# Optimization experiments

Measured on AMD Instinct MI355X. Metric: run time of the kernel, lower is better.

The kernel has to match this reference:

```python
import jax, jax.numpy as jnp
import numpy as np

T, N, M, B = 512, 512, 256, 256

def setup_inputs() -> dict:
    key = jax.random.key(0)
    ks = jax.random.split(key, 6)
    h_t = jax.random.normal(ks[0], (1, B, M), dtype=jnp.float32)
    s_t = jax.random.normal(ks[1], (1, B, M), dtype=jnp.float32)
    data = jax.random.normal(ks[2], (B, T, N), dtype=jnp.float32)
    # torch Linear weight layout: (out_features, in_features)
    W_e = jax.random.normal(ks[3], (T, 2 * M), dtype=jnp.float32) / np.sqrt(2 * M)
    U_e = jax.random.normal(ks[4], (T, T), dtype=jnp.float32) / np.sqrt(T)
    v_e = jax.random.normal(ks[5], (1, T), dtype=jnp.float32) / np.sqrt(T)
    return {"h_t": h_t, "s_t": s_t, "data": data, "W_e": W_e, "U_e": U_e, "v_e": v_e}

def reference(h_t, s_t, data, W_e, U_e, v_e):
    # h_t, s_t: (1, B, m) -> (B, 2m); query is identical across the n repeats,
    # so project once and broadcast instead of materializing (B, n, 2m).
    query = jnp.concatenate([h_t[0], s_t[0]], axis=-1)          # (B, 2m)
    wq = query @ W_e.T                                          # (B, T)
    ud = jnp.einsum('btn,st->bns', data, U_e)                   # (B, n, T)
    alpha = jnp.tanh(wq[:, None, :] + ud)                       # (B, n, T)
    scores = jnp.einsum('bnt,t->bn', alpha, v_e[0])             # (B, n)
    attn = jax.nn.softmax(scores, axis=-1)[:, None, :]          # (B, 1, n)
    return attn
```

## Files before the change

### kernel.cpp

```cpp
#include <hip/hip_runtime.h>
#include <hip/hip_bf16.h>
#include <cmath>

#define T_DIM 512
#define N_DIM 512
#define M_DIM 256
#define B_DIM 256

typedef __bf16 bf16x8 __attribute__((ext_vector_type(8)));
typedef float  f32x4  __attribute__((ext_vector_type(4)));
typedef unsigned int u32;

__device__ __forceinline__ void gload16(const __bf16* g, __bf16* l) {
    __builtin_amdgcn_global_load_lds(
        (const __attribute__((address_space(1))) void*)g,
        (__attribute__((address_space(3))) void*)l, 16, 0, 0);
}

__device__ __forceinline__ int bkey(int r) { return ((r >> 3) ^ (r >> 1)) & 3; }

__global__ __launch_bounds__(256) void uconv_kernel(
    const float* __restrict__ U, __bf16* __restrict__ Uh)
{
    const int i = (blockIdx.x * 256 + threadIdx.x) * 2;
    float2 v = *(const float2*)(U + i);
    Uh[i]   = (__bf16)v.x;
    Uh[i+1] = (__bf16)v.y;
}

__global__ __launch_bounds__(256) void wq_kernel(
    const float* __restrict__ h_t, const float* __restrict__ s_t,
    const float* __restrict__ W_e, float* __restrict__ wq)
{
    __shared__ float q[2 * M_DIM];
    const int b = blockIdx.x;
    const int tid = threadIdx.x;
    q[tid]         = h_t[(size_t)b * M_DIM + tid];
    q[M_DIM + tid] = s_t[(size_t)b * M_DIM + tid];
    __syncthreads();
    for (int tt = tid; tt < T_DIM; tt += 256) {
        const float4* wrow = (const float4*)(W_e + (size_t)tt * (2 * M_DIM));
        float acc = 0.f;
        #pragma unroll 4
        for (int k4 = 0; k4 < (2 * M_DIM) / 4; ++k4) {
            float4 w = wrow[k4];
            acc += q[4*k4+0] * w.x + q[4*k4+1] * w.y
                 + q[4*k4+2] * w.z + q[4*k4+3] * w.w;
        }
        wq[(size_t)b * T_DIM + tt] = acc;
    }
}

__global__ __launch_bounds__(256, 2) void fused7_kernel(
    const float* __restrict__ data, const __bf16* __restrict__ Uh,
    const float* __restrict__ v_e, const float* __restrict__ wq,
    float* __restrict__ partial)
{
    __shared__ __align__(16) __bf16 As[2][128 * 32];
    __shared__ __align__(16) __bf16 Bs[2][256 * 32];
    __shared__ float sc[128];

    const int wg    = blockIdx.x;
    const int xcd   = wg & 7;
    const int local = wg >> 3;
    const int sh    = local & 1;
    const int p     = xcd + 8 * (local >> 1);
    const int b     = p >> 2;
    const int nb    = p & 3;

    const int tid  = threadIdx.x;
    const int lane = tid & 63;
    const int wid  = tid >> 6;
    const int wm   = wid >> 1;
    const int wn   = wid & 1;

    if (tid < 128) sc[tid] = 0.f;

    f32x4 acc[4][8];
    const f32x4 zero = {0.f, 0.f, 0.f, 0.f};
    #pragma unroll
    for (int i = 0; i < 4; ++i)
        #pragma unroll
        for (int j = 0; j < 8; ++j)
            acc[i][j] = zero;

    const float*  Ab = data + (size_t)b * T_DIM * N_DIM + nb * 128;
    const __bf16* Bb = Uh + (size_t)(sh * 256) * T_DIM;

    const int rp = tid >> 4;
    const int cg = tid & 15;
    const int n0 = cg * 8;

    const int r0   = tid >> 2;
    const int keyB = bkey(r0);
    const int ce   = (((tid & 3) ^ keyB) * 8);

    const int fr = lane & 15;
    const int kb = (lane >> 4) * 8;

    int aoff[4];
    #pragma unroll
    for (int mi = 0; mi < 4; ++mi) {
        const int row = wm * 64 + mi * 16 + fr;
        aoff[mi] = row * 32 + (kb ^ (bkey(row) << 3));
    }
    int boff[8];
    #pragma unroll
    for (int ni = 0; ni < 8; ++ni) {
        const int row = wn * 128 + ni * 16 + fr;
        boff[ni] = row * 32 + (kb ^ (bkey(row) << 3));
    }

    const float* s0 = Ab + (size_t)(2 * rp) * N_DIM + n0;
    float4 pa0 = *(const float4*)s0;
    float4 pa1 = *(const float4*)(s0 + 4);
    float4 pa2 = *(const float4*)(s0 + N_DIM);
    float4 pa3 = *(const float4*)(s0 + N_DIM + 4);

    #pragma unroll
    for (int i = 0; i < 4; ++i)
        gload16(Bb + (size_t)(i * 64 + r0) * T_DIM + ce, &Bs[0][tid * 8] + i * 64 * 32);
    {
        u32* As32 = (u32*)As[0];
        const float lo_[8] = {pa0.x, pa0.y, pa0.z, pa0.w, pa1.x, pa1.y, pa1.z, pa1.w};
        const float hi_[8] = {pa2.x, pa2.y, pa2.z, pa2.w, pa3.x, pa3.y, pa3.z, pa3.w};
        #pragma unroll
        for (int j = 0; j < 8; ++j) {
            __bf16 l = (__bf16)lo_[j];
            __bf16 h = (__bf16)hi_[j];
            u32 w = ((u32)__builtin_bit_cast(unsigned short, h) << 16)
                  |  (u32)__builtin_bit_cast(unsigned short, l);
            const int key = (cg ^ (j >> 1)) & 3;
            As32[(n0 + j) * 16 + (rp ^ (key << 2))] = w;
        }
    }
    {
        const float* sn = Ab + (size_t)(32 + 2 * rp) * N_DIM + n0;
        pa0 = *(const float4*)sn;
        pa1 = *(const float4*)(sn + 4);
        pa2 = *(const float4*)(sn + N_DIM);
        pa3 = *(const float4*)(sn + N_DIM + 4);
    }
    __syncthreads();

    int cur = 0;
    for (int k0 = 0; k0 < T_DIM; k0 += 32) {
        bf16x8 a[4], bv[8];
        #pragma unroll
        for (int mi = 0; mi < 4; ++mi)
            a[mi] = *(const bf16x8*)&As[cur][aoff[mi]];
        #pragma unroll
        for (int ni = 0; ni < 8; ++ni)
            bv[ni] = *(const bf16x8*)&Bs[cur][boff[ni]];

        if (k0 + 32 < T_DIM) {
            const int nxt = cur ^ 1;
            #pragma unroll
            for (int i = 0; i < 4; ++i)
                gload16(Bb + (size_t)(i * 64 + r0) * T_DIM + (k0 + 32) + ce,
                        &Bs[nxt][tid * 8] + i * 64 * 32);
            u32* As32 = (u32*)As[nxt];
            const float lo_[8] = {pa0.x, pa0.y, pa0.z, pa0.w, pa1.x, pa1.y, pa1.z, pa1.w};
            const float hi_[8] = {pa2.x, pa2.y, pa2.z, pa2.w, pa3.x, pa3.y, pa3.z, pa3.w};
            #pragma unroll
            for (int j = 0; j < 8; ++j) {
                __bf16 l = (__bf16)lo_[j];
                __bf16 h = (__bf16)hi_[j];
                u32 w = ((u32)__builtin_bit_cast(unsigned short, h) << 16)
                      |  (u32)__builtin_bit_cast(unsigned short, l);
                const int key = (cg ^ (j >> 1)) & 3;
                As32[(n0 + j) * 16 + (rp ^ (key << 2))] = w;
            }
            if (k0 + 64 < T_DIM) {
                const float* sn = Ab + (size_t)(k0 + 64 + 2 * rp) * N_DIM + n0;
                pa0 = *(const float4*)sn;
                pa1 = *(const float4*)(sn + 4);
                pa2 = *(const float4*)(sn + N_DIM);
                pa3 = *(const float4*)(sn + N_DIM + 4);
            }
        }

        __builtin_amdgcn_s_setprio(1);
        #pragma unroll
        for (int mi = 0; mi < 4; ++mi)
            #pragma unroll
            for (int ni = 0; ni < 8; ++ni)
                acc[mi][ni] = __builtin_amdgcn_mfma_f32_16x16x32_bf16(a[mi], bv[ni], acc[mi][ni], 0, 0, 0);
        __builtin_amdgcn_s_setprio(0);

        __syncthreads();
        cur ^= 1;
    }

    float wqv[8], vev[8];
    #pragma unroll
    for (int ni = 0; ni < 8; ++ni) {
        const int scol = sh * 256 + wn * 128 + ni * 16 + fr;
        wqv[ni] = wq[(size_t)b * T_DIM + scol];
        vev[ni] = v_e[scol];
    }
    const int g = lane >> 4;
    #pragma unroll
    for (int mi = 0; mi < 4; ++mi) {
        #pragma unroll
        for (int rg = 0; rg < 4; ++rg) {
            float part = 0.f;
            #pragma unroll
            for (int ni = 0; ni < 8; ++ni)
                part += vev[ni] * tanhf(wqv[ni] + acc[mi][ni][rg]);
            part += __shfl_xor(part, 1);
            part += __shfl_xor(part, 2);
            part += __shfl_xor(part, 4);
            part += __shfl_xor(part, 8);
            if (fr == 0)
                atomicAdd(&sc[wm * 64 + mi * 16 + 4 * g + rg], part);
        }
    }
    __syncthreads();
    if (tid < 128)
        partial[((size_t)b * 2 + sh) * N_DIM + nb * 128 + tid] = sc[tid];
}

__global__ __launch_bounds__(512) void softmax_kernel(
    const float* __restrict__ partial, float* __restrict__ out)
{
    const int b = blockIdx.x;
    const int n = threadIdx.x;
    const float* p = partial + (size_t)b * 2 * N_DIM;
    float s = p[n] + p[N_DIM + n];

    float m = s;
    #pragma unroll
    for (int off = 1; off < 64; off <<= 1)
        m = fmaxf(m, __shfl_xor(m, off));
    __shared__ float red[8];
    const int wv = n >> 6;
    if ((n & 63) == 0) red[wv] = m;
    __syncthreads();
    float bm = red[0];
    #pragma unroll
    for (int i = 1; i < 8; ++i) bm = fmaxf(bm, red[i]);

    float e = expf(s - bm);
    float t = e;
    #pragma unroll
    for (int off = 1; off < 64; off <<= 1)
        t += __shfl_xor(t, off);
    __syncthreads();
    if ((n & 63) == 0) red[wv] = t;
    __syncthreads();
    float tot = 0.f;
    #pragma unroll
    for (int i = 0; i < 8; ++i) tot += red[i];

    out[(size_t)b * N_DIM + n] = e / tot;
}

extern "C" void kernel_launch(void* const* d_in, const int* in_sizes, int n_in,
                              void* d_out, int out_size, void* d_ws, size_t ws_size,
                              hipStream_t stream) {
    const float* h_t  = (const float*)d_in[0];
    const float* s_t  = (const float*)d_in[1];
    const float* data = (const float*)d_in[2];
    const float* W_e  = (const float*)d_in[3];
    const float* U_e  = (const float*)d_in[4];
    const float* v_e  = (const float*)d_in[5];
    float* out = (float*)d_out;

    const size_t wq_elems      = (size_t)B_DIM * T_DIM;
    const size_t partial_elems = (size_t)B_DIM * 2 * N_DIM;
    const size_t u_elems       = (size_t)T_DIM * T_DIM;

    float* wq      = (float*)d_ws;
    float* partial = wq + wq_elems;
    __bf16* Uh     = (__bf16*)(partial + partial_elems);

    wq_kernel<<<B_DIM, 256, 0, stream>>>(h_t, s_t, W_e, wq);
    uconv_kernel<<<(int)(u_elems / 512), 256, 0, stream>>>(U_e, Uh);
    fused7_kernel<<<B_DIM * 8, 256, 0, stream>>>(data, Uh, v_e, wq, partial);
    softmax_kernel<<<B_DIM, 512, 0, stream>>>(partial, out);
}
```

Measured before the change: 175.7 us.

## Make fused GEMM-tanh kernel persistent over four batches and use fast exp tanh

The main kernel now launches 512 workgroups, down from 2048. Each workgroup processes four consecutive batches in one continuous 64-step K loop, so the double-buffered prefetch runs across batch boundaries and the pipeline prologue is amortised. After every 16 steps it runs the tanh/v_e epilogue, writes partial scores, and resets the accumulators and the shared score buffer. tanhf is replaced by an __expf-based formula, which is cheaper but can lose accuracy or overflow to inf for large inputs. The cost is a smaller grid, which may leave compute units underused, and extra barriers inside the loop.

```diff
diff --git a/kernel.cpp b/kernel.cpp
--- a/kernel.cpp
+++ b/kernel.cpp
@@ -18,6 +18,10 @@
 }
 
 __device__ __forceinline__ int bkey(int r) { return ((r >> 3) ^ (r >> 1)) & 3; }
+
+__device__ __forceinline__ float ftanh(float x) {
+    return 1.f - 2.f / (__expf(2.f * x) + 1.f);
+}
 
 __global__ __launch_bounds__(256) void uconv_kernel(
     const float* __restrict__ U, __bf16* __restrict__ Uh)
@@ -51,7 +55,7 @@
     }
 }
 
-__global__ __launch_bounds__(256, 2) void fused7_kernel(
+__global__ __launch_bounds__(256, 2) void fused8_kernel(
     const float* __restrict__ data, const __bf16* __restrict__ Uh,
     const float* __restrict__ v_e, const float* __restrict__ wq,
     float* __restrict__ partial)
@@ -64,9 +68,9 @@
     const int xcd   = wg & 7;
     const int local = wg >> 3;
     const int sh    = local & 1;
-    const int p     = xcd + 8 * (local >> 1);
-    const int b     = p >> 2;
-    const int nb    = p & 3;
+    const int q     = xcd + 8 * (local >> 1);
+    const int bgrp  = q >> 2;
+    const int nb    = q & 3;
 
     const int tid  = threadIdx.x;
     const int lane = tid & 63;
@@ -84,13 +88,13 @@
         for (int j = 0; j < 8; ++j)
             acc[i][j] = zero;
 
-    const float*  Ab = data + (size_t)b * T_DIM * N_DIM + nb * 128;
-    const __bf16* Bb = Uh + (size_t)(sh * 256) * T_DIM;
-
     const int rp = tid >> 4;
     const int cg = tid & 15;
     const int n0 = cg * 8;
 
+    const float* Apan = data + ((size_t)bgrp * 4 * T_DIM) * N_DIM + nb * 128 + n0;
+
+    const __bf16* Bb = Uh + (size_t)(sh * 256) * T_DIM;
     const int r0   = tid >> 2;
     const int keyB = bkey(r0);
     const int ce   = (((tid & 3) ^ keyB) * 8);
@@ -111,12 +115,20 @@
         boff[ni] = row * 32 + (kb ^ (bkey(row) << 3));
     }
 
-    const float* s0 = Ab + (size_t)(2 * rp) * N_DIM + n0;
-    float4 pa0 = *(const float4*)s0;
-    float4 pa1 = *(const float4*)(s0 + 4);
-    float4 pa2 = *(const float4*)(s0 + N_DIM);
-    float4 pa3 = *(const float4*)(s0 + N_DIM + 4);
-
+    float vev[8];
+    #pragma unroll
+    for (int ni = 0; ni < 8; ++ni)
+        vev[ni] = v_e[sh * 256 + wn * 128 + ni * 16 + fr];
+    const int g = lane >> 4;
+
+    float4 pa0, pa1, pa2, pa3;
+    {
+        const float* s0 = Apan + (size_t)(2 * rp) * N_DIM;
+        pa0 = *(const float4*)s0;
+        pa1 = *(const float4*)(s0 + 4);
+        pa2 = *(const float4*)(s0 + N_DIM);
+        pa3 = *(const float4*)(s0 + N_DIM + 4);
+    }
     #pragma unroll
     for (int i = 0; i < 4; ++i)
         gload16(Bb + (size_t)(i * 64 + r0) * T_DIM + ce, &Bs[0][tid * 8] + i * 64 * 32);
@@ -135,7 +147,7 @@
         }
     }
     {
-        const float* sn = Ab + (size_t)(32 + 2 * rp) * N_DIM + n0;
+        const float* sn = Apan + (size_t)(32 + 2 * rp) * N_DIM;
         pa0 = *(const float4*)sn;
         pa1 = *(const float4*)(sn + 4);
         pa2 = *(const float4*)(sn + N_DIM);
@@ -143,8 +155,9 @@
     }
     __syncthreads();
 
-    int cur = 0;
-    for (int k0 = 0; k0 < T_DIM; k0 += 32) {
+    for (int t = 0; t < 64; ++t) {
+        const int cur = t & 1;
+
         bf16x8 a[4], bv[8];
         #pragma unroll
         for (int mi = 0; mi < 4; ++mi)
@@ -153,11 +166,12 @@
         for (int ni = 0; ni < 8; ++ni)
             bv[ni] = *(const bf16x8*)&Bs[cur][boff[ni]];
 
-        if (k0 + 32 < T_DIM) {
+        if (t < 63) {
             const int nxt = cur ^ 1;
+            const int kcol = ((t + 1) & 15) << 5;
             #pragma unroll
             for (int i = 0; i < 4; ++i)
-                gload16(Bb + (size_t)(i * 64 + r0) * T_DIM + (k0 + 32) + ce,
+                gload16(Bb + (size_t)(i * 64 + r0) * T_DIM + kcol + ce,
                         &Bs[nxt][tid * 8] + i * 64 * 32);
             u32* As32 = (u32*)As[nxt];
             const float lo_[8] = {pa0.x, pa0.y, pa0.z, pa0.w, pa1.x, pa1.y, pa1.z, pa1.w};
@@ -171,8 +185,8 @@
                 const int key = (cg ^ (j >> 1)) & 3;
                 As32[(n0 + j) * 16 + (rp ^ (key << 2))] = w;
             }
-            if (k0 + 64 < T_DIM) {
-                const float* sn = Ab + (size_t)(k0 + 64 + 2 * rp) * N_DIM + n0;
+            if (t < 62) {
+                const float* sn = Apan + (size_t)(32 * (t + 2) + 2 * rp) * N_DIM;
                 pa0 = *(const float4*)sn;
                 pa1 = *(const float4*)(sn + 4);
                 pa2 = *(const float4*)(sn + N_DIM);
@@ -189,36 +203,42 @@
         __builtin_amdgcn_s_setprio(0);
 
         __syncthreads();
-        cur ^= 1;
-    }
-
-    float wqv[8], vev[8];
-    #pragma unroll
-    for (int ni = 0; ni < 8; ++ni) {
-        const int scol = sh * 256 + wn * 128 + ni * 16 + fr;
-        wqv[ni] = wq[(size_t)b * T_DIM + scol];
-        vev[ni] = v_e[scol];
-    }
-    const int g = lane >> 4;
-    #pragma unroll
-    for (int mi = 0; mi < 4; ++mi) {
-        #pragma unroll
-        for (int rg = 0; rg < 4; ++rg) {
-            float part = 0.f;
+
+        if ((t & 15) == 15) {
+            const int b = bgrp * 4 + (t >> 4);
+            float wqv[8];
             #pragma unroll
             for (int ni = 0; ni < 8; ++ni)
-                part += vev[ni] * tanhf(wqv[ni] + acc[mi][ni][rg]);
-            part += __shfl_xor(part, 1);
-            part += __shfl_xor(part, 2);
-            part += __shfl_xor(part, 4);
-            part += __shfl_xor(part, 8);
-            if (fr == 0)
-                atomicAdd(&sc[wm * 64 + mi * 16 + 4 * g + rg], part);
+                wqv[ni] = wq[(size_t)b * T_DIM + sh * 256 + wn * 128 + ni * 16 + fr];
+            #pragma unroll
+            for (int mi = 0; mi < 4; ++mi) {
+                #pragma unroll
+                for (int rg = 0; rg < 4; ++rg) {
+                    float part = 0.f;
+                    #pragma unroll
+                    for (int ni = 0; ni < 8; ++ni)
+                        part += vev[ni] * ftanh(wqv[ni] + acc[mi][ni][rg]);
+                    part += __shfl_xor(part, 1);
+                    part += __shfl_xor(part, 2);
+                    part += __shfl_xor(part, 4);
+                    part += __shfl_xor(part, 8);
+                    if (fr == 0)
+                        atomicAdd(&sc[wm * 64 + mi * 16 + 4 * g + rg], part);
+                }
+            }
+            __syncthreads();
+            if (tid < 128)
+                partial[((size_t)b * 2 + sh) * N_DIM + nb * 128 + tid] = sc[tid];
+            if (t < 63) {
+                if (tid < 128) sc[tid] = 0.f;
+                #pragma unroll
+                for (int i = 0; i < 4; ++i)
+                    #pragma unroll
+                    for (int j = 0; j < 8; ++j)
+                        acc[i][j] = zero;
+            }
         }
     }
-    __syncthreads();
-    if (tid < 128)
-        partial[((size_t)b * 2 + sh) * N_DIM + nb * 128 + tid] = sc[tid];
 }
 
 __global__ __launch_bounds__(512) void softmax_kernel(
@@ -277,6 +297,6 @@
 
     wq_kernel<<<B_DIM, 256, 0, stream>>>(h_t, s_t, W_e, wq);
     uconv_kernel<<<(int)(u_elems / 512), 256, 0, stream>>>(U_e, Uh);
-    fused7_kernel<<<B_DIM * 8, 256, 0, stream>>>(data, Uh, v_e, wq, partial);
+    fused8_kernel<<<512, 256, 0, stream>>>(data, Uh, v_e, wq, partial);
     softmax_kernel<<<B_DIM, 512, 0, stream>>>(partial, out);
 }
```

Result: faster. 164.7 us (-6.3%).
